# Optimization experiments

Measured on AMD Instinct MI355X. Metric: run time of the kernel, lower is better.

Reference implementation:

```python
import jax, jax.numpy as jnp
import numpy as np

N = 50000      # nodes
E = 800000     # edges
D = 128        # d_model
H = 8          # heads
DH = D // H    # head dim
FF = 512       # dim_ff
NB = 32        # degree buckets
EPS = 1e-5


def _ln(x, g, b):
    mu = jnp.mean(x, axis=-1, keepdims=True)
    var = jnp.mean((x - mu) ** 2, axis=-1, keepdims=True)
    return (x - mu) * jax.lax.rsqrt(var + EPS) * g + b


def setup_inputs() -> dict:
    key = jax.random.key(0)
    ks = jax.random.split(key, 12)
    s = 0.02
    return {
        'x': jax.random.normal(ks[0], (N, D), jnp.float32),
        'row': jnp.sort(jax.random.randint(ks[1], (E,), 0, N, jnp.int32)),
        'col': jax.random.randint(ks[2], (E,), 0, N, jnp.int32),
        'deg_bucket': jax.random.randint(ks[3], (N,), 0, NB, jnp.int32),
        'Wq': jax.random.normal(ks[4], (D, D), jnp.float32) * s,
        'bq': jnp.zeros((D,), jnp.float32),
        'Wk': jax.random.normal(ks[5], (D, D), jnp.float32) * s,
        'bk': jnp.zeros((D,), jnp.float32),
        'Wv': jax.random.normal(ks[6], (D, D), jnp.float32) * s,
        'bv': jnp.zeros((D,), jnp.float32),
        'Wo': jax.random.normal(ks[7], (D, D), jnp.float32) * s,
        'bo': jnp.zeros((D,), jnp.float32),
        'emb': jax.random.normal(ks[8], (NB, H), jnp.float32) * s,
        'ln1_g': jnp.ones((D,), jnp.float32), 'ln1_b': jnp.zeros((D,), jnp.float32),
        'ln2_g': jnp.ones((D,), jnp.float32), 'ln2_b': jnp.zeros((D,), jnp.float32),
        'W1': jax.random.normal(ks[9], (D, FF), jnp.float32) * s,
        'b1': jnp.zeros((FF,), jnp.float32),
        'W2': jax.random.normal(ks[10], (FF, D), jnp.float32) * s,
        'b2': jnp.zeros((D,), jnp.float32),
    }


def reference(x, row, col, deg_bucket, Wq, bq, Wk, bk, Wv, bv, Wo, bo, emb,
              ln1_g, ln1_b, ln2_g, ln2_b, W1, b1, W2, b2):
    scale = DH ** (-0.5)
    Q = (x @ Wq + bq).reshape(N, H, DH)
    K = (x @ Wk + bk).reshape(N, H, DH)
    V = (x @ Wv + bv).reshape(N, H, DH)
    # edge-wise QK dot products: [E, H]
    scores = jnp.einsum('ehd,ehd->eh', Q[row], K[col]) * scale
    scores = scores + emb[deg_bucket[row]] + emb[deg_bucket[col]]
    # segment softmax over destination node `row`
    max_s = jax.ops.segment_max(scores, row, num_segments=N, indices_are_sorted=True)
    exp_s = jnp.exp(scores - max_s[row])
    sum_s = jax.ops.segment_sum(exp_s, row, num_segments=N, indices_are_sorted=True)
    alpha = exp_s / jnp.maximum(sum_s[row], 1e-12)
    # scatter-weighted aggregation of V[col]: [N, H, DH]
    agg = jax.ops.segment_sum(alpha[..., None] * V[col], row, num_segments=N,
                              indices_are_sorted=True)
    out = agg.reshape(N, D) @ Wo + bo
    h = _ln(x + out, ln1_g, ln1_b)
    ffo = jax.nn.gelu(h @ W1 + b1, approximate=False) @ W2 + b2
    return _ln(h + ffo, ln2_g, ln2_b)
```

## Files before the change

kernel.cpp:

```cpp
#include <hip/hip_runtime.h>
#include <math.h>

#define NN 50000
#define NE 800000
#define DM 128
#define NH 8
#define FF 512
#define NBLK 391
#define NBLK64 782

#define PB_X    6250
#define PB_WT   192
#define PB_RP   196
#define PB_EMB  1563
#define PB_TOT  (PB_X + PB_WT + PB_RP + PB_EMB)

typedef __attribute__((ext_vector_type(8))) short bf16x8;
typedef __attribute__((ext_vector_type(4))) float f32x4;
typedef __attribute__((ext_vector_type(2))) float f32x2;

__device__ __forceinline__ short f2bf(float f) {
    union { float f; unsigned u; } v; v.f = f;
    unsigned r = v.u + 0x7fff + ((v.u >> 16) & 1);
    return (short)(r >> 16);
}
__device__ __forceinline__ float bf2f(short s) {
    union { unsigned u; float f; } v; v.u = ((unsigned)(unsigned short)s) << 16;
    return v.f;
}
__device__ __forceinline__ unsigned char f2fp8(float f) {
    int p = __builtin_amdgcn_cvt_pk_fp8_f32(f, f, 0, false);
    return (unsigned char)(p & 0xff);
}

__device__ __forceinline__ float gelu_f(float x) {
    float u = x * (0.7978845608f + 0.0356774081f * x * x);
    float t = 1.f - 2.f / (__expf(2.f * u) + 1.f);
    return 0.5f * x * (1.f + t);
}

__device__ __forceinline__ void gload16(const void* g, void* l) {
    __builtin_amdgcn_global_load_lds(
        (const __attribute__((address_space(1))) void*)g,
        (__attribute__((address_space(3))) void*)l, 16, 0, 0);
}

template <int R>
__device__ __forceinline__ void stage_tile_f8(const unsigned char* __restrict__ src,
                                              int row0, int maxrow, int ld, int col0,
                                              unsigned char* sm) {
    const int tid = threadIdx.x;
    const int w = tid >> 6, l = tid & 63;
    const int p = l & 7;
    const int rsub = l >> 3;
    #pragma unroll
    for (int j = 0; j < (R >> 5); ++j) {
        int lr = w * (R >> 2) + j * 8 + rsub;
        int gr = row0 + lr; gr = gr > maxrow ? maxrow : gr;
        int g = p ^ (lr & 7);
        const unsigned char* gp = src + (size_t)gr * ld + col0 + g * 16;
        gload16(gp, sm + (w * (R >> 2) + j * 8) * 128);
    }
}

__device__ __forceinline__ long frag_ld_f8(const unsigned char* sm, int outer, int slot) {
    return *(const long*)(sm + outer * 128 +
                          (((slot >> 1) ^ (outer & 7)) << 4) + ((slot & 1) << 3));
}

__device__ __forceinline__ void mfma_tile128_f8(const unsigned char* sA,
                                                const unsigned char* sB,
                                                int wm, int wn, int lane,
                                                f32x4 acc[4][4]) {
    const int l15 = lane & 15, l4 = lane >> 4;
    #pragma unroll
    for (int ks = 0; ks < 4; ++ks) {
        long a[4], b[4];
        int slot = ks * 4 + l4;
        #pragma unroll
        for (int f = 0; f < 4; ++f) a[f] = frag_ld_f8(sA, wm * 64 + f * 16 + l15, slot);
        #pragma unroll
        for (int f = 0; f < 4; ++f) b[f] = frag_ld_f8(sB, wn * 64 + f * 16 + l15, slot);
        #pragma unroll
        for (int fm = 0; fm < 4; ++fm)
            #pragma unroll
            for (int fn = 0; fn < 4; ++fn)
                acc[fm][fn] = __builtin_amdgcn_mfma_f32_16x16x32_fp8_fp8(
                    a[fm], b[fn], acc[fm][fn], 0, 0, 0);
    }
}

__device__ __forceinline__ void mfma_tile64_f8(const unsigned char* sA,
                                               const unsigned char* sB,
                                               int wm, int wn, int lane,
                                               f32x4 acc[2][4]) {
    const int l15 = lane & 15, l4 = lane >> 4;
    #pragma unroll
    for (int ks = 0; ks < 4; ++ks) {
        long a[2], b[4];
        int slot = ks * 4 + l4;
        #pragma unroll
        for (int f = 0; f < 2; ++f) a[f] = frag_ld_f8(sA, wm * 32 + f * 16 + l15, slot);
        #pragma unroll
        for (int f = 0; f < 4; ++f) b[f] = frag_ld_f8(sB, wn * 64 + f * 16 + l15, slot);
        #pragma unroll
        for (int fm = 0; fm < 2; ++fm)
            #pragma unroll
            for (int fn = 0; fn < 4; ++fn)
                acc[fm][fn] = __builtin_amdgcn_mfma_f32_16x16x32_fp8_fp8(
                    a[fm], b[fn], acc[fm][fn], 0, 0, 0);
    }
}

__global__ __launch_bounds__(256) void k_prep(
    const float* __restrict__ x, short* __restrict__ xb,
    unsigned char* __restrict__ xb8,
    const float* __restrict__ Wq, const float* __restrict__ Wk,
    const float* __restrict__ Wv, const float* __restrict__ Wo,
    const float* __restrict__ W1, const float* __restrict__ W2,
    unsigned char* __restrict__ wqkvo,
    unsigned char* __restrict__ w1f8, unsigned char* __restrict__ w2f8,
    const int* __restrict__ row, int* __restrict__ rowptr,
    const int* __restrict__ db, const float* __restrict__ emb,
    float* __restrict__ embn)
{
    int bid = blockIdx.x;
    const int tid = threadIdx.x;

    if (bid < PB_X) {
        int i = bid * 256 + tid;
        if (i < NN * DM / 4) {
            float4 v = ((const float4*)x)[i];
            ((short4*)xb)[i] = make_short4(f2bf(v.x), f2bf(v.y), f2bf(v.z), f2bf(v.w));
            ((uchar4*)xb8)[i] = make_uchar4(f2fp8(v.x), f2fp8(v.y), f2fp8(v.z), f2fp8(v.w));
        }
        return;
    }
    bid -= PB_X;
    if (bid < PB_WT) {
        const float* W; int K, N, bx, by;
        unsigned char* Wf8;
        if (bid < 64) {
            int wsel = bid >> 4, rel = bid & 15;
            W = wsel == 0 ? Wq : wsel == 1 ? Wk : wsel == 2 ? Wv : Wo;
            Wf8 = wqkvo + wsel * 16384; K = 128; N = 128; bx = rel & 3; by = rel >> 2;
        } else if (bid < 128) {
            int rel = bid - 64;
            W = W1; Wf8 = w1f8; K = 128; N = 512; bx = rel & 15; by = rel >> 4;
        } else {
            int rel = bid - 128;
            W = W2; Wf8 = w2f8; K = 512; N = 128; bx = rel & 3; by = rel >> 2;
        }
        __shared__ float t[32][33];
        int n0 = bx * 32, k0 = by * 32;
        int r = tid >> 3, c4 = (tid & 7) * 4;
        float4 v = *(const float4*)(W + (size_t)(k0 + r) * N + n0 + c4);
        t[r][c4 + 0] = v.x; t[r][c4 + 1] = v.y; t[r][c4 + 2] = v.z; t[r][c4 + 3] = v.w;
        __syncthreads();
        uchar4 o = make_uchar4(f2fp8(16.f * t[c4 + 0][r]), f2fp8(16.f * t[c4 + 1][r]),
                               f2fp8(16.f * t[c4 + 2][r]), f2fp8(16.f * t[c4 + 3][r]));
        *(uchar4*)(Wf8 + (size_t)(n0 + r) * K + k0 + c4) = o;
        return;
    }
    bid -= PB_WT;
    if (bid < PB_RP) {
        int n = bid * 256 + tid;
        if (n > NN) return;
        int lo = 0, hi = NE;
        while (lo < hi) {
            int mid = (lo + hi) >> 1;
            if (row[mid] < n) lo = mid + 1; else hi = mid;
        }
        rowptr[n] = lo;
        return;
    }
    bid -= PB_RP;
    {
        int i = bid * 256 + tid;
        if (i < NN * NH) embn[i] = emb[db[i >> 3] * NH + (i & 7)];
    }
}

__global__ __launch_bounds__(256) void k_gemm_qkv(
    const unsigned char* __restrict__ xb8, const unsigned char* __restrict__ wqkvo,
    const float* __restrict__ bq, const float* __restrict__ bk,
    const float* __restrict__ bv,
    short* __restrict__ Qb, unsigned char* __restrict__ Kf8,
    unsigned char* __restrict__ Vf8)
{
    __shared__ unsigned char smA[16384];
    __shared__ unsigned char smB[16384];
    const int tid = threadIdx.x, lane = tid & 63, wid = tid >> 6;
    const int wm = wid >> 1, wn = wid & 1;
    const int r0 = blockIdx.x * 128;

    stage_tile_f8<128>(xb8, r0, NN - 1, 128, 0, smA);
    #pragma unroll
    for (int m = 0; m < 3; ++m) {
        if (m) __syncthreads();
        stage_tile_f8<128>(wqkvo + m * 16384, 0, 127, 128, 0, smB);
        __syncthreads();
        f32x4 acc[4][4];
        #pragma unroll
        for (int i = 0; i < 4; ++i)
            #pragma unroll
            for (int j = 0; j < 4; ++j)
                acc[i][j] = (f32x4){0.f, 0.f, 0.f, 0.f};
        mfma_tile128_f8(smA, smB, wm, wn, lane, acc);

        const float* bias = m == 0 ? bq : (m == 1 ? bk : bv);
        #pragma unroll
        for (int fn = 0; fn < 4; ++fn) {
            int col = wn * 64 + fn * 16 + (lane & 15);
            float bc = bias[col];
            #pragma unroll
            for (int fm = 0; fm < 4; ++fm) {
                int rowb = r0 + wm * 64 + fm * 16 + (lane >> 4) * 4;
                #pragma unroll
                for (int rr = 0; rr < 4; ++rr) {
                    int gr = rowb + rr;
                    if (gr < NN) {
                        float v = acc[fm][fn][rr] * 0.0625f + bc;
                        if (m == 0)
                            Qb[(size_t)gr * DM + col] = f2bf(v);
                        else if (m == 1)
                            Kf8[(size_t)gr * DM + col] = f2fp8(v);
                        else
                            Vf8[(size_t)gr * DM + col] = f2fp8(v);
                    }
                }
            }
        }
    }
}

__global__ __launch_bounds__(256) void k_attn_wave(
    const short* __restrict__ Qb, const unsigned char* __restrict__ Kf8,
    const unsigned char* __restrict__ Vf8, const int* __restrict__ col,
    const int* __restrict__ rowptr, const float* __restrict__ embn,
    unsigned char* __restrict__ agg8)
{
    const int lane = threadIdx.x & 63;
    const int n = blockIdx.x * 4 + (threadIdx.x >> 6);
    const int e0 = rowptr[n], e1 = rowptr[n + 1];
    const int s = lane >> 3, h = lane & 7;
    const int h2 = lane >> 3;

    f32x2 qf2[8];
    {
        const bf16x8* qp = (const bf16x8*)(Qb + (size_t)n * DM + h * 16);
        bf16x8 q0 = qp[0], q1 = qp[1];
        #pragma unroll
        for (int j = 0; j < 4; ++j) {
            qf2[j] = (f32x2){bf2f(q0[2 * j]), bf2f(q0[2 * j + 1])};
            qf2[4 + j] = (f32x2){bf2f(q1[2 * j]), bf2f(q1[2 * j + 1])};
        }
    }
    const float embr = embn[(size_t)n * NH + h];

    float m = -INFINITY, l = 0.f;
    f32x2 accv = (f32x2){0.f, 0.f};

    for (int c0 = e0; c0 < e1; c0 += 16) {
        int ea = c0 + s, eb = c0 + 8 + s;
        bool va = ea < e1, vb = eb < e1;
        int ca = col[va ? ea : e1 - 1];
        int cb = col[vb ? eb : e1 - 1];

        int4 kwa = *(const int4*)(Kf8 + (size_t)ca * DM + h * 16);
        int4 kwb = *(const int4*)(Kf8 + (size_t)cb * DM + h * 16);
        float ema = embn[(size_t)ca * NH + h];
        float emB = embn[(size_t)cb * NH + h];

        int nv = e1 - c0; nv = nv > 16 ? 16 : nv;
        unsigned short vv[16];
        #pragma unroll
        for (int j = 0; j < 8; ++j) {
            int cj = __shfl(ca, j * 8);
            vv[j] = (j < nv) ? *(const unsigned short*)(Vf8 + (size_t)cj * DM + lane * 2) : 0;
        }
        #pragma unroll
        for (int j = 0; j < 8; ++j) {
            int cj = __shfl(cb, j * 8);
            vv[8 + j] = (8 + j < nv) ? *(const unsigned short*)(Vf8 + (size_t)cj * DM + lane * 2) : 0;
        }

        f32x2 da2 = (f32x2){0.f, 0.f}, db2 = (f32x2){0.f, 0.f};
        {
            int ka[4] = {kwa.x, kwa.y, kwa.z, kwa.w};
            int kb[4] = {kwb.x, kwb.y, kwb.z, kwb.w};
            #pragma unroll
            for (int w = 0; w < 4; ++w) {
                f32x2 alo = __builtin_amdgcn_cvt_pk_f32_fp8(ka[w], false);
                f32x2 ahi = __builtin_amdgcn_cvt_pk_f32_fp8(ka[w], true);
                f32x2 blo = __builtin_amdgcn_cvt_pk_f32_fp8(kb[w], false);
                f32x2 bhi = __builtin_amdgcn_cvt_pk_f32_fp8(kb[w], true);
                da2 += qf2[2 * w] * alo + qf2[2 * w + 1] * ahi;
                db2 += qf2[2 * w] * blo + qf2[2 * w + 1] * bhi;
            }
        }
        float da = da2[0] + da2[1];
        float dbv = db2[0] + db2[1];
        float sa = va ? da * 0.25f + embr + ema : -INFINITY;
        float sb = vb ? dbv * 0.25f + embr + emB : -INFINITY;

        float mc = fmaxf(sa, sb);
        mc = fmaxf(mc, __shfl_xor(mc, 8));
        mc = fmaxf(mc, __shfl_xor(mc, 16));
        mc = fmaxf(mc, __shfl_xor(mc, 32));
        float mn = fmaxf(m, mc);
        float f = __expf(m - mn);
        m = mn;
        float pa = __expf(sa - mn);
        float pb = __expf(sb - mn);
        float ps = pa + pb;
        ps += __shfl_xor(ps, 8);
        ps += __shfl_xor(ps, 16);
        ps += __shfl_xor(ps, 32);
        l = l * f + ps;

        float fr = __shfl(f, h2);
        accv *= (f32x2){fr, fr};
        #pragma unroll
        for (int j = 0; j < 8; ++j) {
            float pj = __shfl(pa, j * 8 + h2);
            f32x2 vd = __builtin_amdgcn_cvt_pk_f32_fp8((int)vv[j], false);
            accv += (f32x2){pj, pj} * vd;
        }
        #pragma unroll
        for (int j = 0; j < 8; ++j) {
            float pj = __shfl(pb, j * 8 + h2);
            f32x2 vd = __builtin_amdgcn_cvt_pk_f32_fp8((int)vv[8 + j], false);
            accv += (f32x2){pj, pj} * vd;
        }
    }
    float la = __shfl(l, h2);
    la = fmaxf(la, 1e-12f);
    int p = __builtin_amdgcn_cvt_pk_fp8_f32(16.f * accv[0] / la,
                                            16.f * accv[1] / la, 0, false);
    *(unsigned short*)(agg8 + (size_t)n * DM + lane * 2) = (unsigned short)p;
}

__global__ __launch_bounds__(256) void k_gemm_ln1(
    const unsigned char* __restrict__ agg8, const unsigned char* __restrict__ Wof8,
    const float* __restrict__ bo, const short* __restrict__ xbr,
    const float* __restrict__ g, const float* __restrict__ b,
    short* __restrict__ hb, unsigned char* __restrict__ hb8)
{
    __shared__ union {
        struct { unsigned char A[16384]; unsigned char B[16384]; } s;
        float hs[128 * 129];
    } u;
    __shared__ float mu[128], rsd[128];
    const int tid = threadIdx.x, lane = tid & 63, wid = tid >> 6;
    const int wm = wid >> 1, wn = wid & 1;
    const int r0 = blockIdx.x * 128;

    stage_tile_f8<128>(agg8, r0, NN - 1, 128, 0, u.s.A);
    stage_tile_f8<128>(Wof8, 0, 127, 128, 0, u.s.B);
    __syncthreads();

    f32x4 acc[4][4];
    #pragma unroll
    for (int i = 0; i < 4; ++i)
        #pragma unroll
        for (int j = 0; j < 4; ++j) acc[i][j] = (f32x4){0.f, 0.f, 0.f, 0.f};
    mfma_tile128_f8(u.s.A, u.s.B, wm, wn, lane, acc);
    __syncthreads();

    #pragma unroll
    for (int fn = 0; fn < 4; ++fn) {
        int col = wn * 64 + fn * 16 + (lane & 15);
        float bc = bo[col];
        #pragma unroll
        for (int fm = 0; fm < 4; ++fm) {
            int rowb = wm * 64 + fm * 16 + (lane >> 4) * 4;
            #pragma unroll
            for (int rr = 0; rr < 4; ++rr) {
                int r_ = rowb + rr, gr = r0 + r_;
                float xr = (gr < NN) ? bf2f(xbr[(size_t)gr * DM + col]) : 0.f;
                u.hs[r_ * 129 + col] = acc[fm][fn][rr] * (1.f / 256.f) + bc + xr;
            }
        }
    }
    __syncthreads();

    {
        int rrow = tid >> 1, half = tid & 1;
        float s = 0.f, q = 0.f;
        #pragma unroll 8
        for (int c = 0; c < 64; ++c) {
            float v = u.hs[rrow * 129 + half * 64 + c];
            s += v; q += v * v;
        }
        s += __shfl_xor(s, 1);
        q += __shfl_xor(q, 1);
        float m = s * (1.f / DM);
        float var = q * (1.f / DM) - m * m;
        if (half == 0) { mu[rrow] = m; rsd[rrow] = rsqrtf(var + 1e-5f); }
    }
    __syncthreads();

    for (int i = 0; i < 64; ++i) {
        int idx = i * 256 + tid;
        int rrow = idx >> 7, c = idx & 127;
        int gr = r0 + rrow;
        if (gr < NN) {
            float v = (u.hs[rrow * 129 + c] - mu[rrow]) * rsd[rrow] * g[c] + b[c];
            hb[(size_t)gr * DM + c] = f2bf(v);
            hb8[(size_t)gr * DM + c] = f2fp8(v);
        }
    }
}

__global__ __launch_bounds__(256) void k_ffn_fused(
    const unsigned char* __restrict__ hb8, const unsigned char* __restrict__ W1f8,
    const float* __restrict__ b1, const unsigned char* __restrict__ W2f8,
    const float* __restrict__ b2, const short* __restrict__ hb,
    const float* __restrict__ g, const float* __restrict__ bb,
    float* __restrict__ out)
{
    extern __shared__ char smraw[];
    unsigned char* A = (unsigned char*)smraw;
    unsigned char* B = A + 8192;
    unsigned char* C = B + 16384;
    float* hs = (float*)smraw;
    __shared__ float mu[64], rsd[64];

    const int tid = threadIdx.x, lane = tid & 63, wid = tid >> 6;
    const int wm = wid >> 1, wn = wid & 1;
    const int l15 = lane & 15, l4 = lane >> 4;
    const int r0 = blockIdx.x * 64;

    f32x4 acc2[2][4];
    #pragma unroll
    for (int i = 0; i < 2; ++i)
        #pragma unroll
        for (int j = 0; j < 4; ++j) acc2[i][j] = (f32x4){0.f, 0.f, 0.f, 0.f};

    stage_tile_f8<64>(hb8, r0, NN - 1, 128, 0, A);

    for (int kc = 0; kc < 4; ++kc) {
        if (kc) __syncthreads();
        stage_tile_f8<128>(W1f8, kc * 128, FF - 1, 128, 0, B);
        __syncthreads();

        f32x4 accf[2][4];
        #pragma unroll
        for (int i = 0; i < 2; ++i)
            #pragma unroll
            for (int j = 0; j < 4; ++j) accf[i][j] = (f32x4){0.f, 0.f, 0.f, 0.f};
        mfma_tile64_f8(A, B, wm, wn, lane, accf);

        #pragma unroll
        for (int fn = 0; fn < 4; ++fn) {
            int nloc = wn * 64 + fn * 16 + l15;
            float bc = b1[kc * 128 + nloc];
            #pragma unroll
            for (int fm = 0; fm < 2; ++fm) {
                int rowb = wm * 32 + fm * 16 + l4 * 4;
                #pragma unroll
                for (int rr = 0; rr < 4; ++rr) {
                    int row = rowb + rr;
                    float v = 16.f * gelu_f(accf[fm][fn][rr] * 0.0625f + bc);
                    C[row * 128 + ((((nloc >> 4) ^ (row & 7)) << 4) | (nloc & 15))]
                        = f2fp8(v);
                }
            }
        }
        __syncthreads();
        stage_tile_f8<128>(W2f8, 0, 127, 512, kc * 128, B);
        __syncthreads();
        mfma_tile64_f8(C, B, wm, wn, lane, acc2);
    }
    __syncthreads();

    #pragma unroll
    for (int fn = 0; fn < 4; ++fn) {
        int col = wn * 64 + fn * 16 + l15;
        float bc = b2[col];
        #pragma unroll
        for (int fm = 0; fm < 2; ++fm) {
            int rowb = wm * 32 + fm * 16 + l4 * 4;
            #pragma unroll
            for (int rr = 0; rr < 4; ++rr) {
                int r_ = rowb + rr, gr = r0 + r_;
                int cr = gr < NN ? gr : NN - 1;
                float hr = bf2f(hb[(size_t)cr * DM + col]);
                hs[r_ * 129 + col] = acc2[fm][fn][rr] * (1.f / 256.f) + bc + hr;
            }
        }
    }
    __syncthreads();

    {
        int rrow = tid >> 2, q = tid & 3;
        float s = 0.f, qq = 0.f;
        #pragma unroll 8
        for (int c = 0; c < 32; ++c) {
            float v = hs[rrow * 129 + q * 32 + c];
            s += v; qq += v * v;
        }
        s += __shfl_xor(s, 1);  qq += __shfl_xor(qq, 1);
        s += __shfl_xor(s, 2);  qq += __shfl_xor(qq, 2);
        float m = s * (1.f / DM);
        float var = qq * (1.f / DM) - m * m;
        if (q == 0) { mu[rrow] = m; rsd[rrow] = rsqrtf(var + 1e-5f); }
    }
    __syncthreads();

    for (int i = 0; i < 32; ++i) {
        int idx = i * 256 + tid;
        int rrow = idx >> 7, c = idx & 127;
        int gr = r0 + rrow;
        if (gr < NN)
            out[(size_t)gr * DM + c] =
                (hs[rrow * 129 + c] - mu[rrow]) * rsd[rrow] * g[c] + bb[c];
    }
}

extern "C" void kernel_launch(void* const* d_in, const int* in_sizes, int n_in,
                              void* d_out, int out_size, void* d_ws, size_t ws_size,
                              hipStream_t stream) {
    const float* x   = (const float*)d_in[0];
    const int* row   = (const int*)d_in[1];
    const int* col   = (const int*)d_in[2];
    const int* db    = (const int*)d_in[3];
    const float* Wq  = (const float*)d_in[4];
    const float* bq  = (const float*)d_in[5];
    const float* Wk  = (const float*)d_in[6];
    const float* bk  = (const float*)d_in[7];
    const float* Wv  = (const float*)d_in[8];
    const float* bv  = (const float*)d_in[9];
    const float* Wo  = (const float*)d_in[10];
    const float* bo  = (const float*)d_in[11];
    const float* emb = (const float*)d_in[12];
    const float* g1  = (const float*)d_in[13];
    const float* b1n = (const float*)d_in[14];
    const float* g2  = (const float*)d_in[15];
    const float* b2n = (const float*)d_in[16];
    const float* W1  = (const float*)d_in[17];
    const float* b1  = (const float*)d_in[18];
    const float* W2  = (const float*)d_in[19];
    const float* b2  = (const float*)d_in[20];

    char* W = (char*)d_ws;
    float* embn          = (float*)(W + 0);
    unsigned char* Kf8   = (unsigned char*)(W + 1600000);
    unsigned char* Vf8   = (unsigned char*)(W + 8000000);
    unsigned char* xb8   = (unsigned char*)(W + 14400000);
    unsigned char* agg8  = (unsigned char*)(W + 20800000);
    short* xb     = (short*)(W + 38400000);
    short* Qb     = (short*)(W + 51200000);
    short* hb     = (short*)(W + 51200000);
    unsigned char* hb8 = (unsigned char*)(W + 76800000);
    unsigned char* wqkvo = (unsigned char*)(W + 89600000);
    unsigned char* w1f8  = (unsigned char*)(W + 89665536);
    unsigned char* w2f8  = (unsigned char*)(W + 89731072);
    int* rowptr   = (int*)(W + 89796608);

    k_prep<<<PB_TOT, 256, 0, stream>>>(x, xb, xb8, Wq, Wk, Wv, Wo, W1, W2,
                                       wqkvo, w1f8, w2f8, row, rowptr, db, emb, embn);
    k_gemm_qkv<<<NBLK, 256, 0, stream>>>(xb8, wqkvo, bq, bk, bv, Qb, Kf8, Vf8);
    k_attn_wave<<<NN / 4, 256, 0, stream>>>(Qb, Kf8, Vf8, col, rowptr, embn, agg8);
    k_gemm_ln1<<<NBLK, 256, 0, stream>>>(agg8, wqkvo + 49152, bo, xb, g1, b1n, hb, hb8);
    k_ffn_fused<<<NBLK64, 256, 33024, stream>>>(hb8, w1f8, b1, w2f8, b2, hb,
                                                g2, b2n, (float*)d_out);
}
```

Measured before the change: 179.3 us.

## Compute FFN epilogue LayerNorm in registers with shuffle row reductions

The FFN kernel's final residual add and LayerNorm now stay in MFMA accumulator registers. Row sums are reduced with cross-lane shuffles and a small per-wave-column shared stats array, replacing the 33KB shared-memory staging of the full output tile and the separate reduction pass. This drops a barrier and the LDS round trip and lets shared memory shrink to static arrays, which may raise occupancy. It also packs GELU outputs with the hardware fp8 pack conversion, and the output stores become strided 16-column writes per lane rather than fully coalesced rows.

```diff
diff --git a/kernel.cpp b/kernel.cpp
--- a/kernel.cpp
+++ b/kernel.cpp
@@ -420,13 +420,10 @@
     const float* __restrict__ g, const float* __restrict__ bb,
     float* __restrict__ out)
 {
-    extern __shared__ char smraw[];
-    unsigned char* A = (unsigned char*)smraw;
-    unsigned char* B = A + 8192;
-    unsigned char* C = B + 16384;
-    float* hs = (float*)smraw;
-    __shared__ float mu[64], rsd[64];
-
+    __shared__ unsigned char A[8192];
+    __shared__ unsigned char B[16384];
+    __shared__ unsigned char C[8192];
+    __shared__ float2 rowstat[2][64];
     const int tid = threadIdx.x, lane = tid & 63, wid = tid >> 6;
     const int wm = wid >> 1, wn = wid & 1;
     const int l15 = lane & 15, l4 = lane >> 4;
@@ -456,16 +453,22 @@
         for (int fn = 0; fn < 4; ++fn) {
             int nloc = wn * 64 + fn * 16 + l15;
             float bc = b1[kc * 128 + nloc];
+            int coff = (((nloc >> 4) ^ 0) << 4);
+            (void)coff;
             #pragma unroll
             for (int fm = 0; fm < 2; ++fm) {
                 int rowb = wm * 32 + fm * 16 + l4 * 4;
-                #pragma unroll
-                for (int rr = 0; rr < 4; ++rr) {
-                    int row = rowb + rr;
-                    float v = 16.f * gelu_f(accf[fm][fn][rr] * 0.0625f + bc);
-                    C[row * 128 + ((((nloc >> 4) ^ (row & 7)) << 4) | (nloc & 15))]
-                        = f2fp8(v);
-                }
+                float v0 = 16.f * gelu_f(accf[fm][fn][0] * 0.0625f + bc);
+                float v1 = 16.f * gelu_f(accf[fm][fn][1] * 0.0625f + bc);
+                float v2 = 16.f * gelu_f(accf[fm][fn][2] * 0.0625f + bc);
+                float v3 = 16.f * gelu_f(accf[fm][fn][3] * 0.0625f + bc);
+                int p01 = __builtin_amdgcn_cvt_pk_fp8_f32(v0, v1, 0, false);
+                int p23 = __builtin_amdgcn_cvt_pk_fp8_f32(v2, v3, 0, false);
+                int row0_ = rowb + 0, row1_ = rowb + 1, row2_ = rowb + 2, row3_ = rowb + 3;
+                C[row0_ * 128 + ((((nloc >> 4) ^ (row0_ & 7)) << 4) | (nloc & 15))] = (unsigned char)(p01 & 0xff);
+                C[row1_ * 128 + ((((nloc >> 4) ^ (row1_ & 7)) << 4) | (nloc & 15))] = (unsigned char)((p01 >> 8) & 0xff);
+                C[row2_ * 128 + ((((nloc >> 4) ^ (row2_ & 7)) << 4) | (nloc & 15))] = (unsigned char)(p23 & 0xff);
+                C[row3_ * 128 + ((((nloc >> 4) ^ (row3_ & 7)) << 4) | (nloc & 15))] = (unsigned char)((p23 >> 8) & 0xff);
             }
         }
         __syncthreads();
@@ -473,49 +476,65 @@
         __syncthreads();
         mfma_tile64_f8(C, B, wm, wn, lane, acc2);
     }
+
+    float b2c[4];
+    #pragma unroll
+    for (int fn = 0; fn < 4; ++fn) b2c[fn] = b2[wn * 64 + fn * 16 + l15];
+
+    float srow[2][4], qrow[2][4];
+    #pragma unroll
+    for (int fm = 0; fm < 2; ++fm) {
+        #pragma unroll
+        for (int rr = 0; rr < 4; ++rr) {
+            int ml = wm * 32 + fm * 16 + l4 * 4 + rr;
+            int gr = r0 + ml;
+            int cr = gr < NN ? gr : NN - 1;
+            float s = 0.f, ss = 0.f;
+            #pragma unroll
+            for (int fn = 0; fn < 4; ++fn) {
+                int colc = wn * 64 + fn * 16 + l15;
+                float hr = bf2f(hb[(size_t)cr * DM + colc]);
+                float v = acc2[fm][fn][rr] * (1.f / 256.f) + b2c[fn] + hr;
+                acc2[fm][fn][rr] = v;
+                s += v; ss += v * v;
+            }
+            s += __shfl_xor(s, 1);  ss += __shfl_xor(ss, 1);
+            s += __shfl_xor(s, 2);  ss += __shfl_xor(ss, 2);
+            s += __shfl_xor(s, 4);  ss += __shfl_xor(ss, 4);
+            s += __shfl_xor(s, 8);  ss += __shfl_xor(ss, 8);
+            srow[fm][rr] = s; qrow[fm][rr] = ss;
+        }
+    }
+    if (l15 == 0) {
+        #pragma unroll
+        for (int fm = 0; fm < 2; ++fm)
+            #pragma unroll
+            for (int rr = 0; rr < 4; ++rr)
+                rowstat[wn][wm * 32 + fm * 16 + l4 * 4 + rr] =
+                    make_float2(srow[fm][rr], qrow[fm][rr]);
+    }
     __syncthreads();
 
     #pragma unroll
-    for (int fn = 0; fn < 4; ++fn) {
-        int col = wn * 64 + fn * 16 + l15;
-        float bc = b2[col];
-        #pragma unroll
-        for (int fm = 0; fm < 2; ++fm) {
-            int rowb = wm * 32 + fm * 16 + l4 * 4;
-            #pragma unroll
-            for (int rr = 0; rr < 4; ++rr) {
-                int r_ = rowb + rr, gr = r0 + r_;
-                int cr = gr < NN ? gr : NN - 1;
-                float hr = bf2f(hb[(size_t)cr * DM + col]);
-                hs[r_ * 129 + col] = acc2[fm][fn][rr] * (1.f / 256.f) + bc + hr;
+    for (int fm = 0; fm < 2; ++fm) {
+        #pragma unroll
+        for (int rr = 0; rr < 4; ++rr) {
+            int ml = wm * 32 + fm * 16 + l4 * 4 + rr;
+            int gr = r0 + ml;
+            float2 a0 = rowstat[0][ml], a1 = rowstat[1][ml];
+            float s = a0.x + a1.x, ss = a0.y + a1.y;
+            float mu = s * (1.f / DM);
+            float var = ss * (1.f / DM) - mu * mu;
+            float rs = rsqrtf(var + 1e-5f);
+            if (gr < NN) {
+                #pragma unroll
+                for (int fn = 0; fn < 4; ++fn) {
+                    int colc = wn * 64 + fn * 16 + l15;
+                    out[(size_t)gr * DM + colc] =
+                        (acc2[fm][fn][rr] - mu) * rs * g[colc] + bb[colc];
+                }
             }
         }
-    }
-    __syncthreads();
-
-    {
-        int rrow = tid >> 2, q = tid & 3;
-        float s = 0.f, qq = 0.f;
-        #pragma unroll 8
-        for (int c = 0; c < 32; ++c) {
-            float v = hs[rrow * 129 + q * 32 + c];
-            s += v; qq += v * v;
-        }
-        s += __shfl_xor(s, 1);  qq += __shfl_xor(qq, 1);
-        s += __shfl_xor(s, 2);  qq += __shfl_xor(qq, 2);
-        float m = s * (1.f / DM);
-        float var = qq * (1.f / DM) - m * m;
-        if (q == 0) { mu[rrow] = m; rsd[rrow] = rsqrtf(var + 1e-5f); }
-    }
-    __syncthreads();
-
-    for (int i = 0; i < 32; ++i) {
-        int idx = i * 256 + tid;
-        int rrow = idx >> 7, c = idx & 127;
-        int gr = r0 + rrow;
-        if (gr < NN)
-            out[(size_t)gr * DM + c] =
-                (hs[rrow * 129 + c] - mu[rrow]) * rsd[rrow] * g[c] + bb[c];
     }
 }
 
@@ -564,6 +583,6 @@
     k_gemm_qkv<<<NBLK, 256, 0, stream>>>(xb8, wqkvo, bq, bk, bv, Qb, Kf8, Vf8);
     k_attn_wave<<<NN / 4, 256, 0, stream>>>(Qb, Kf8, Vf8, col, rowptr, embn, agg8);
     k_gemm_ln1<<<NBLK, 256, 0, stream>>>(agg8, wqkvo + 49152, bo, xb, g1, b1n, hb, hb8);
-    k_ffn_fused<<<NBLK64, 256, 33024, stream>>>(hb8, w1f8, b1, w2f8, b2, hb,
-                                                g2, b2n, (float*)d_out);
-}
+    k_ffn_fused<<<NBLK64, 256, 0, stream>>>(hb8, w1f8, b1, w2f8, b2, hb,
+                                            g2, b2n, (float*)d_out);
+}
```

After: 179.6 us. No clear change (+0.1%).
